# Performance work log

Hardware: AMD Instinct MI355X
Metric: run time of the kernel (lower is better)

Reference implementation:

```python
import jax, jax.numpy as jnp
import numpy as np

H = 6            # nheads
DPH = 200.0      # dim_per_head buffer = mha_dimension / nheads (used as divisor, NOT sqrt)
EPS = 1e-5


def layernorm(x, g, b):
    m = jnp.mean(x, axis=-1, keepdims=True)
    v = jnp.mean((x - m) ** 2, axis=-1, keepdims=True)
    return (x - m) * jax.lax.rsqrt(v + EPS) * g + b


def leaky(x):
    # torch.nn.LeakyReLU(True) -> negative_slope = 1.0 (identity), kept for faithfulness
    return jnp.where(x >= 0, x, 1.0 * x)


def setup_inputs() -> dict:
    key = jax.random.key(0)
    ks = jax.random.split(key, 16)
    B, L, D, M = 4, 2048, 512, 1200
    s_in = 1.0 / np.sqrt(D)
    s_m = 1.0 / np.sqrt(M)
    return {
        "query": jax.random.normal(ks[0], (B, L, D), jnp.float32),
        "keyval": jax.random.normal(ks[1], (B, 1, D), jnp.float32),
        "Wq": jax.random.normal(ks[2], (D, M), jnp.float32) * s_in,
        "bq": jnp.zeros((M,), jnp.float32),
        "Wkv": jax.random.normal(ks[3], (D, 2 * M), jnp.float32) * s_in,
        "bkv": jnp.zeros((2 * M,), jnp.float32),
        "Wff": jax.random.normal(ks[4], (M, D), jnp.float32) * s_m,
        "bff": jnp.zeros((D,), jnp.float32),
        "g1": jnp.ones((D,), jnp.float32),
        "b1": jnp.zeros((D,), jnp.float32),
        "W2a": jax.random.normal(ks[5], (D, 4 * D), jnp.float32) * s_in,
        "b2a": jnp.zeros((4 * D,), jnp.float32),
        "W2b": jax.random.normal(ks[6], (4 * D, D), jnp.float32) / np.sqrt(4 * D),
        "b2b": jnp.zeros((D,), jnp.float32),
        "g2": jnp.ones((D,), jnp.float32),
        "b2": jnp.zeros((D,), jnp.float32),
    }


def reference(query, keyval, Wq, bq, Wkv, bkv, Wff, bff, g1, b1,
              W2a, b2a, W2b, b2b, g2, b2):
    B, L, D = query.shape
    kv = jnp.broadcast_to(keyval, query.shape)           # keyval.expand_as(query)
    Q = query @ Wq + bq                                  # [B,L,M]
    KV = kv @ Wkv + bkv                                  # [B,L,2M]
    K, V = jnp.split(KV, 2, axis=-1)

    def heads(x):  # b l (h d) -> b h l d
        return x.reshape(B, L, H, -1).transpose(0, 2, 1, 3)

    Qh, Kh, Vh = heads(Q), heads(K), heads(V)
    logits = jnp.einsum('bhid,bhjd->bhij', Qh, Kh) / DPH  # note: / d, not / sqrt(d)
    sm = jax.nn.softmax(logits, axis=-1)                  # [B,H,L,L]
    mha = jnp.einsum('bhij,bhjd->bhid', sm, Vh)
    mha_ = mha.transpose(0, 2, 1, 3).reshape(B, L, -1)    # b h i d -> b i (h d)

    out = mha_ @ Wff + bff                                # dropout = identity (eval)
    out_ = layernorm(out + query, g1, b1)
    out2 = leaky(out_ @ W2a + b2a) @ W2b + b2b
    out3 = layernorm(out_ + out2, g2, b2)
    out3 = out3 + kv
    return out3, sm
```

## Files before the change

### kernel.cpp

```cpp
#include <hip/hip_runtime.h>
#include <hip/hip_bf16.h>


typedef __bf16 bf16x8 __attribute__((ext_vector_type(8)));
typedef float f32x4 __attribute__((ext_vector_type(4)));

constexpr size_t OUT3_N = 4ull * 2048 * 512;
constexpr size_t SM_N   = 4ull * 6 * 2048 * 2048;

__global__ __launch_bounds__(256) void prep_k(const float* __restrict__ W2a,
        const float* __restrict__ b2a, __bf16* __restrict__ A1,
        const float* __restrict__ W2b, __bf16* __restrict__ W2bT){
    const int bid = blockIdx.x, tid = threadIdx.x;
    if (bid < 1152){
        int r = bid >> 1;
        int c = (bid & 1) * 1024 + tid * 4;
        float4 v;
        if (r < 512)       v = *(const float4*)(W2a + (size_t)r * 2048 + c);
        else if (r == 512) v = *(const float4*)(b2a + c);
        else               v = make_float4(0.f, 0.f, 0.f, 0.f);
        __bf16* o = A1 + (size_t)r * 2048 + c;
        o[0] = (__bf16)v.x; o[1] = (__bf16)v.y; o[2] = (__bf16)v.z; o[3] = (__bf16)v.w;
    } else {
        __shared__ float tile[32][33];
        int t = bid - 1152;
        int c0 = (t & 15) * 32, r0 = (t >> 4) * 32;
        int tx = tid & 31, ty = tid >> 5;
        for (int i = ty; i < 32; i += 8)
            tile[i][tx] = W2b[(size_t)(r0 + i) * 512 + c0 + tx];
        __syncthreads();
        for (int i = ty; i < 32; i += 8)
            W2bT[(size_t)(c0 + i) * 2048 + r0 + tx] = (__bf16)tile[tx][i];
    }
}

__global__ void tcast_k(const float* __restrict__ in, __bf16* __restrict__ out, int R, int C){
    __shared__ float tile[32][33];
    int c0 = blockIdx.x * 32, r0 = blockIdx.y * 32;
    int tx = threadIdx.x, ty = threadIdx.y;
    for (int i = ty; i < 32; i += 8)
        tile[i][tx] = in[(size_t)(r0 + i) * C + c0 + tx];
    __syncthreads();
    for (int i = ty; i < 32; i += 8)
        out[(size_t)(c0 + i) * R + r0 + tx] = (__bf16)tile[tx][i];
}

__global__ void kv_k(const float* __restrict__ keyval, const float* __restrict__ Wkv,
                     const float* __restrict__ bkv, float* __restrict__ V){
    int b = blockIdx.x, m = blockIdx.y * 256 + threadIdx.x, kc = blockIdx.z;
    if (m >= 1200) return;
    float acc = (kc == 0) ? bkv[1200 + m] : 0.f;
    const float* kvb = keyval + (size_t)b * 512;
    int d0 = kc * 64;
    #pragma unroll 8
    for (int d = d0; d < d0 + 64; ++d)
        acc += kvb[d] * Wkv[(size_t)d * 2400 + 1200 + m];
    atomicAdd(&V[b * 1200 + m], acc);
}

__global__ void oc_k(const float* __restrict__ V, const float* __restrict__ Wff,
                     const float* __restrict__ bff, float* __restrict__ oc){
    int b = blockIdx.x, j = blockIdx.y * 256 + threadIdx.x, kc = blockIdx.z;
    float acc = (kc == 0) ? bff[j] : 0.f;
    const float* vb = V + b * 1200;
    int m0 = kc * 100;
    #pragma unroll 5
    for (int m = m0; m < m0 + 100; ++m)
        acc += vb[m] * Wff[(size_t)m * 512 + j];
    atomicAdd(&oc[b * 512 + j], acc);
}

__global__ __launch_bounds__(256) void ln1_k(const float* __restrict__ q,
        const float* __restrict__ oc, const float* __restrict__ g1,
        const float* __restrict__ b1, __bf16* __restrict__ Xb){
    const int rid = blockIdx.x;
    const int b = rid >> 11;
    const int t = threadIdx.x;
    const size_t base = (size_t)rid * 512;
    float2 qv = *(const float2*)(q + base + 2 * t);
    float2 ov = *(const float2*)(oc + (size_t)b * 512 + 2 * t);
    float v0 = qv.x + ov.x, v1 = qv.y + ov.y;
    float s = v0 + v1, ss = v0 * v0 + v1 * v1;
    for (int off = 32; off; off >>= 1){ s += __shfl_down(s, off); ss += __shfl_down(ss, off); }
    __shared__ float red[8];
    int wv = t >> 6, ln = t & 63;
    if (ln == 0){ red[wv] = s; red[4 + wv] = ss; }
    __syncthreads();
    if (t == 0){
        float S  = red[0] + red[1] + red[2] + red[3];
        float SS = red[4] + red[5] + red[6] + red[7];
        float m = S * (1.0f / 512.0f);
        float var = SS * (1.0f / 512.0f) - m * m;
        red[0] = m; red[1] = rsqrtf(var + 1e-5f);
    }
    __syncthreads();
    float m = red[0], r = red[1];
    float2 gv = *(const float2*)(g1 + 2 * t);
    float2 bv = *(const float2*)(b1 + 2 * t);
    union { __bf16 h[2]; unsigned u; } pk;
    pk.h[0] = (__bf16)((v0 - m) * r * gv.x + bv.x);
    pk.h[1] = (__bf16)((v1 - m) * r * gv.y + bv.y);
    *(unsigned*)(Xb + base + 2 * t) = pk.u;
}

__global__ __launch_bounds__(256) void ln2_k(const __bf16* __restrict__ X,
        const float* __restrict__ o2, const float* __restrict__ bfrow,
        const float* __restrict__ b2b, const float* __restrict__ g2,
        const float* __restrict__ b2, const float* __restrict__ keyval,
        float* __restrict__ out3){
    const int rid = blockIdx.x;
    const int b = rid >> 11;
    const int t = threadIdx.x;
    const size_t base = (size_t)rid * 512;
    union { unsigned u; __bf16 h[2]; } xv;
    xv.u = *(const unsigned*)(X + base + 2 * t);
    float2 cv = *(const float2*)(o2 + base + 2 * t);
    float f0 = bfrow[2 * t] + b2b[2 * t], f1 = bfrow[2 * t + 1] + b2b[2 * t + 1];
    float v0 = (float)xv.h[0] + cv.x + f0, v1 = (float)xv.h[1] + cv.y + f1;
    float s = v0 + v1, ss = v0 * v0 + v1 * v1;
    for (int off = 32; off; off >>= 1){ s += __shfl_down(s, off); ss += __shfl_down(ss, off); }
    __shared__ float red[8];
    int wv = t >> 6, ln = t & 63;
    if (ln == 0){ red[wv] = s; red[4 + wv] = ss; }
    __syncthreads();
    if (t == 0){
        float S  = red[0] + red[1] + red[2] + red[3];
        float SS = red[4] + red[5] + red[6] + red[7];
        float m = S * (1.0f / 512.0f);
        float var = SS * (1.0f / 512.0f) - m * m;
        red[0] = m; red[1] = rsqrtf(var + 1e-5f);
    }
    __syncthreads();
    float m = red[0], r = red[1];
    float2 gv = *(const float2*)(g2 + 2 * t);
    float2 bv = *(const float2*)(b2 + 2 * t);
    float2 kv = *(const float2*)(keyval + (size_t)b * 512 + 2 * t);
    float y0 = (v0 - m) * r * gv.x + bv.x + kv.x;
    float y1 = (v1 - m) * r * gv.y + bv.y + kv.y;
    *(float2*)(out3 + base + 2 * t) = make_float2(y0, y1);
}

__global__ __launch_bounds__(256) void gemm_bt_k(const __bf16* __restrict__ A,
        const __bf16* __restrict__ BT, float* __restrict__ C, int Ndim, int Kdim){
    __shared__ __bf16 As[64 * 64];
    __shared__ __bf16 Bs[64 * 64];
    const int tid = threadIdx.x, wave = tid >> 6, lane = tid & 63;
    const int bm = blockIdx.x * 64, bn = blockIdx.y * 64;
    const int r_st = wave * 8 + (lane >> 3);
    const int c8g  = (lane & 7) ^ (r_st & 7);
    const __bf16* Ag = A  + (size_t)(bm + r_st) * Kdim + c8g * 8;
    const __bf16* Bg = BT + (size_t)(bn + r_st) * Kdim + c8g * 8;
    const size_t rowskip = (size_t)32 * Kdim;
    const int wm = (wave >> 1) * 32, wn = (wave & 1) * 32;
    const int lm = lane & 15, lq = lane >> 4;
    f32x4 acc[2][2] = {};
    for (int k0 = 0; k0 < Kdim; k0 += 64){
        __builtin_amdgcn_global_load_lds(
            (const __attribute__((address_space(1))) void*)(Ag + k0),
            (__attribute__((address_space(3))) void*)&As[wave * 512], 16, 0, 0);
        __builtin_amdgcn_global_load_lds(
            (const __attribute__((address_space(1))) void*)(Ag + k0 + rowskip),
            (__attribute__((address_space(3))) void*)&As[2048 + wave * 512], 16, 0, 0);
        __builtin_amdgcn_global_load_lds(
            (const __attribute__((address_space(1))) void*)(Bg + k0),
            (__attribute__((address_space(3))) void*)&Bs[wave * 512], 16, 0, 0);
        __builtin_amdgcn_global_load_lds(
            (const __attribute__((address_space(1))) void*)(Bg + k0 + rowskip),
            (__attribute__((address_space(3))) void*)&Bs[2048 + wave * 512], 16, 0, 0);
        __syncthreads();
        #pragma unroll
        for (int kb = 0; kb < 64; kb += 32){
            const int sw = (((kb >> 3) + lq) ^ (lm & 7)) << 3;
            bf16x8 a0 = *(const bf16x8*)&As[(wm + lm) * 64 + sw];
            bf16x8 a1 = *(const bf16x8*)&As[(wm + 16 + lm) * 64 + sw];
            bf16x8 b0 = *(const bf16x8*)&Bs[(wn + lm) * 64 + sw];
            bf16x8 b1 = *(const bf16x8*)&Bs[(wn + 16 + lm) * 64 + sw];
            acc[0][0] = __builtin_amdgcn_mfma_f32_16x16x32_bf16(a0, b0, acc[0][0], 0, 0, 0);
            acc[0][1] = __builtin_amdgcn_mfma_f32_16x16x32_bf16(a0, b1, acc[0][1], 0, 0, 0);
            acc[1][0] = __builtin_amdgcn_mfma_f32_16x16x32_bf16(a1, b0, acc[1][0], 0, 0, 0);
            acc[1][1] = __builtin_amdgcn_mfma_f32_16x16x32_bf16(a1, b1, acc[1][1], 0, 0, 0);
        }
        __syncthreads();
    }
    for (int mi = 0; mi < 2; ++mi)
      for (int ni = 0; ni < 2; ++ni)
        for (int r = 0; r < 4; ++r){
            int row = bm + wm + mi * 16 + lq * 4 + r;
            int col = bn + wn + ni * 16 + lm;
            C[(size_t)row * Ndim + col] = acc[mi][ni][r];
        }
}

__global__ void fill_k(float4* __restrict__ p, size_t n4, float val){
    size_t i = (size_t)blockIdx.x * blockDim.x + threadIdx.x;
    size_t stride = (size_t)gridDim.x * blockDim.x;
    float4 v = make_float4(val, val, val, val);
    for (; i < n4; i += stride) p[i] = v;
}

extern "C" void kernel_launch(void* const* d_in, const int* in_sizes, int n_in,
                              void* d_out, int out_size, void* d_ws, size_t ws_size,
                              hipStream_t stream){
    const float* query  = (const float*)d_in[0];
    const float* keyval = (const float*)d_in[1];
    const float* Wkv = (const float*)d_in[4];
    const float* bkv = (const float*)d_in[5];
    const float* Wff = (const float*)d_in[6];
    const float* bff = (const float*)d_in[7];
    const float* g1  = (const float*)d_in[8];
    const float* b1  = (const float*)d_in[9];
    const float* W2a = (const float*)d_in[10];
    const float* b2a = (const float*)d_in[11];
    const float* W2b = (const float*)d_in[12];
    const float* b2b = (const float*)d_in[13];
    const float* g2  = (const float*)d_in[14];
    const float* b2  = (const float*)d_in[15];

    float* out3 = (float*)d_out;
    float* smf  = out3 + OUT3_N;

    char* base = (ws_size >= (64ull << 20)) ? (char*)d_ws : (char*)smf;
    float*  t_Wf   = (float*)base;
    float*  t_out2 = t_Wf + 294912;
    float*  t_V    = t_out2 + 4194304;
    float*  t_oc   = t_V + 4800;
    __bf16* t_A1   = (__bf16*)(t_oc + 2048);
    __bf16* t_W2bT = t_A1 + 1179648;
    __bf16* t_WfT  = t_W2bT + 1048576;
    __bf16* t_X    = t_WfT + 262144;

    hipMemsetAsync(t_V, 0, (4800 + 2048) * sizeof(float), stream);
    prep_k<<<2176, 256, 0, stream>>>(W2a, b2a, t_A1, W2b, t_W2bT);
    kv_k<<<dim3(4, 5, 8), 256, 0, stream>>>(keyval, Wkv, bkv, t_V);
    oc_k<<<dim3(4, 2, 12), 256, 0, stream>>>(t_V, Wff, bff, t_oc);
    gemm_bt_k<<<dim3(9, 8), 256, 0, stream>>>(t_A1, t_W2bT, t_Wf, 512, 2048);
    tcast_k<<<dim3(16, 16), dim3(32, 8), 0, stream>>>(t_Wf, t_WfT, 512, 512);
    ln1_k<<<8192, 256, 0, stream>>>(query, t_oc, g1, b1, t_X);
    gemm_bt_k<<<dim3(128, 8), 256, 0, stream>>>(t_X, t_WfT, t_out2, 512, 512);
    ln2_k<<<8192, 256, 0, stream>>>(t_X, t_out2, t_Wf + 294912 - 512, b2b, g2, b2, keyval, out3);
    fill_k<<<4096, 256, 0, stream>>>((float4*)smf, SM_N / 4, 1.0f / 2048.0f);
}
```

Baseline: 542.8 us.

## Fuse softmax fill slices into each stage kernel and split-K the weight-fold GEMM

The big constant fill of the softmax output is split into six slices. Each slice is appended as extra blocks to one of the pipeline kernels, so the bandwidth-bound fill overlaps with the small compute stages instead of running alone at the end. The fill uses non-temporal stores. Several small kernels are merged: kv goes into prep, tcast into ln1. The 576x512x2048 fold GEMM is split along K four ways with atomic accumulation into a zeroed buffer to use more CUs. It also now reads the correct bias row of the folded weight. In exchange, fill blocks compete with compute blocks for CUs, and the atomics add contention.

```diff
diff --git a/kernel.cpp b/kernel.cpp
--- a/kernel.cpp
+++ b/kernel.cpp
@@ -6,146 +6,32 @@
 typedef float f32x4 __attribute__((ext_vector_type(4)));
 
 constexpr size_t OUT3_N = 4ull * 2048 * 512;
-constexpr size_t SM_N   = 4ull * 6 * 2048 * 2048;
-
-__global__ __launch_bounds__(256) void prep_k(const float* __restrict__ W2a,
-        const float* __restrict__ b2a, __bf16* __restrict__ A1,
-        const float* __restrict__ W2b, __bf16* __restrict__ W2bT){
-    const int bid = blockIdx.x, tid = threadIdx.x;
-    if (bid < 1152){
-        int r = bid >> 1;
-        int c = (bid & 1) * 1024 + tid * 4;
-        float4 v;
-        if (r < 512)       v = *(const float4*)(W2a + (size_t)r * 2048 + c);
-        else if (r == 512) v = *(const float4*)(b2a + c);
-        else               v = make_float4(0.f, 0.f, 0.f, 0.f);
-        __bf16* o = A1 + (size_t)r * 2048 + c;
-        o[0] = (__bf16)v.x; o[1] = (__bf16)v.y; o[2] = (__bf16)v.z; o[3] = (__bf16)v.w;
-    } else {
-        __shared__ float tile[32][33];
-        int t = bid - 1152;
-        int c0 = (t & 15) * 32, r0 = (t >> 4) * 32;
-        int tx = tid & 31, ty = tid >> 5;
-        for (int i = ty; i < 32; i += 8)
-            tile[i][tx] = W2b[(size_t)(r0 + i) * 512 + c0 + tx];
-        __syncthreads();
-        for (int i = ty; i < 32; i += 8)
-            W2bT[(size_t)(c0 + i) * 2048 + r0 + tx] = (__bf16)tile[tx][i];
-    }
-}
-
-__global__ void tcast_k(const float* __restrict__ in, __bf16* __restrict__ out, int R, int C){
-    __shared__ float tile[32][33];
-    int c0 = blockIdx.x * 32, r0 = blockIdx.y * 32;
-    int tx = threadIdx.x, ty = threadIdx.y;
-    for (int i = ty; i < 32; i += 8)
-        tile[i][tx] = in[(size_t)(r0 + i) * C + c0 + tx];
-    __syncthreads();
-    for (int i = ty; i < 32; i += 8)
-        out[(size_t)(c0 + i) * R + r0 + tx] = (__bf16)tile[tx][i];
-}
-
-__global__ void kv_k(const float* __restrict__ keyval, const float* __restrict__ Wkv,
-                     const float* __restrict__ bkv, float* __restrict__ V){
-    int b = blockIdx.x, m = blockIdx.y * 256 + threadIdx.x, kc = blockIdx.z;
-    if (m >= 1200) return;
-    float acc = (kc == 0) ? bkv[1200 + m] : 0.f;
-    const float* kvb = keyval + (size_t)b * 512;
-    int d0 = kc * 64;
-    #pragma unroll 8
-    for (int d = d0; d < d0 + 64; ++d)
-        acc += kvb[d] * Wkv[(size_t)d * 2400 + 1200 + m];
-    atomicAdd(&V[b * 1200 + m], acc);
-}
-
-__global__ void oc_k(const float* __restrict__ V, const float* __restrict__ Wff,
-                     const float* __restrict__ bff, float* __restrict__ oc){
-    int b = blockIdx.x, j = blockIdx.y * 256 + threadIdx.x, kc = blockIdx.z;
-    float acc = (kc == 0) ? bff[j] : 0.f;
-    const float* vb = V + b * 1200;
-    int m0 = kc * 100;
-    #pragma unroll 5
-    for (int m = m0; m < m0 + 100; ++m)
-        acc += vb[m] * Wff[(size_t)m * 512 + j];
-    atomicAdd(&oc[b * 512 + j], acc);
-}
-
-__global__ __launch_bounds__(256) void ln1_k(const float* __restrict__ q,
-        const float* __restrict__ oc, const float* __restrict__ g1,
-        const float* __restrict__ b1, __bf16* __restrict__ Xb){
-    const int rid = blockIdx.x;
-    const int b = rid >> 11;
-    const int t = threadIdx.x;
-    const size_t base = (size_t)rid * 512;
-    float2 qv = *(const float2*)(q + base + 2 * t);
-    float2 ov = *(const float2*)(oc + (size_t)b * 512 + 2 * t);
-    float v0 = qv.x + ov.x, v1 = qv.y + ov.y;
-    float s = v0 + v1, ss = v0 * v0 + v1 * v1;
-    for (int off = 32; off; off >>= 1){ s += __shfl_down(s, off); ss += __shfl_down(ss, off); }
-    __shared__ float red[8];
-    int wv = t >> 6, ln = t & 63;
-    if (ln == 0){ red[wv] = s; red[4 + wv] = ss; }
-    __syncthreads();
-    if (t == 0){
-        float S  = red[0] + red[1] + red[2] + red[3];
-        float SS = red[4] + red[5] + red[6] + red[7];
-        float m = S * (1.0f / 512.0f);
-        float var = SS * (1.0f / 512.0f) - m * m;
-        red[0] = m; red[1] = rsqrtf(var + 1e-5f);
-    }
-    __syncthreads();
-    float m = red[0], r = red[1];
-    float2 gv = *(const float2*)(g1 + 2 * t);
-    float2 bv = *(const float2*)(b1 + 2 * t);
-    union { __bf16 h[2]; unsigned u; } pk;
-    pk.h[0] = (__bf16)((v0 - m) * r * gv.x + bv.x);
-    pk.h[1] = (__bf16)((v1 - m) * r * gv.y + bv.y);
-    *(unsigned*)(Xb + base + 2 * t) = pk.u;
-}
-
-__global__ __launch_bounds__(256) void ln2_k(const __bf16* __restrict__ X,
-        const float* __restrict__ o2, const float* __restrict__ bfrow,
-        const float* __restrict__ b2b, const float* __restrict__ g2,
-        const float* __restrict__ b2, const float* __restrict__ keyval,
-        float* __restrict__ out3){
-    const int rid = blockIdx.x;
-    const int b = rid >> 11;
-    const int t = threadIdx.x;
-    const size_t base = (size_t)rid * 512;
-    union { unsigned u; __bf16 h[2]; } xv;
-    xv.u = *(const unsigned*)(X + base + 2 * t);
-    float2 cv = *(const float2*)(o2 + base + 2 * t);
-    float f0 = bfrow[2 * t] + b2b[2 * t], f1 = bfrow[2 * t + 1] + b2b[2 * t + 1];
-    float v0 = (float)xv.h[0] + cv.x + f0, v1 = (float)xv.h[1] + cv.y + f1;
-    float s = v0 + v1, ss = v0 * v0 + v1 * v1;
-    for (int off = 32; off; off >>= 1){ s += __shfl_down(s, off); ss += __shfl_down(ss, off); }
-    __shared__ float red[8];
-    int wv = t >> 6, ln = t & 63;
-    if (ln == 0){ red[wv] = s; red[4 + wv] = ss; }
-    __syncthreads();
-    if (t == 0){
-        float S  = red[0] + red[1] + red[2] + red[3];
-        float SS = red[4] + red[5] + red[6] + red[7];
-        float m = S * (1.0f / 512.0f);
-        float var = SS * (1.0f / 512.0f) - m * m;
-        red[0] = m; red[1] = rsqrtf(var + 1e-5f);
-    }
-    __syncthreads();
-    float m = red[0], r = red[1];
-    float2 gv = *(const float2*)(g2 + 2 * t);
-    float2 bv = *(const float2*)(b2 + 2 * t);
-    float2 kv = *(const float2*)(keyval + (size_t)b * 512 + 2 * t);
-    float y0 = (v0 - m) * r * gv.x + bv.x + kv.x;
-    float y1 = (v1 - m) * r * gv.y + bv.y + kv.y;
-    *(float2*)(out3 + base + 2 * t) = make_float2(y0, y1);
-}
-
-__global__ __launch_bounds__(256) void gemm_bt_k(const __bf16* __restrict__ A,
-        const __bf16* __restrict__ BT, float* __restrict__ C, int Ndim, int Kdim){
+constexpr size_t SM_N4  = (4ull * 6 * 2048 * 2048) / 4;
+constexpr float  SMV    = 1.0f / 2048.0f;
+
+constexpr size_t S1 = 0,        C1 = 6291456;
+constexpr size_t S2 = 6291456,  C2 = 4194304;
+constexpr size_t S3 = 10485760, C3 = 6291456;
+constexpr size_t S4 = 16777216, C4 = 3145728;
+constexpr size_t S5 = 19922944, C5 = 2621440;
+constexpr size_t S6 = 22544384, C6 = 2621440;
+static_assert(S6 + C6 == SM_N4, "fill slices must cover sm");
+
+__device__ inline void fill_slice(f32x4* __restrict__ p, size_t base, size_t cnt,
+                                  int fb, int nfb){
+    const f32x4 v = { SMV, SMV, SMV, SMV };
+    const size_t stride = (size_t)nfb * 256;
+    for (size_t j = (size_t)fb * 256 + threadIdx.x; j < cnt; j += stride)
+        __builtin_nontemporal_store(v, p + base + j);
+}
+
+template<bool ATOMIC>
+__device__ void gemm_tile(const __bf16* __restrict__ A, const __bf16* __restrict__ BT,
+                          float* __restrict__ C, int Ndim, int Kdim,
+                          int bm, int bn, int k0beg, int k0end){
     __shared__ __bf16 As[64 * 64];
     __shared__ __bf16 Bs[64 * 64];
     const int tid = threadIdx.x, wave = tid >> 6, lane = tid & 63;
-    const int bm = blockIdx.x * 64, bn = blockIdx.y * 64;
     const int r_st = wave * 8 + (lane >> 3);
     const int c8g  = (lane & 7) ^ (r_st & 7);
     const __bf16* Ag = A  + (size_t)(bm + r_st) * Kdim + c8g * 8;
@@ -154,7 +40,7 @@
     const int wm = (wave >> 1) * 32, wn = (wave & 1) * 32;
     const int lm = lane & 15, lq = lane >> 4;
     f32x4 acc[2][2] = {};
-    for (int k0 = 0; k0 < Kdim; k0 += 64){
+    for (int k0 = k0beg; k0 < k0end; k0 += 64){
         __builtin_amdgcn_global_load_lds(
             (const __attribute__((address_space(1))) void*)(Ag + k0),
             (__attribute__((address_space(3))) void*)&As[wave * 512], 16, 0, 0);
@@ -182,20 +68,187 @@
         }
         __syncthreads();
     }
+    #pragma unroll
     for (int mi = 0; mi < 2; ++mi)
+      #pragma unroll
       for (int ni = 0; ni < 2; ++ni)
+        #pragma unroll
         for (int r = 0; r < 4; ++r){
             int row = bm + wm + mi * 16 + lq * 4 + r;
             int col = bn + wn + ni * 16 + lm;
-            C[(size_t)row * Ndim + col] = acc[mi][ni][r];
-        }
-}
-
-__global__ void fill_k(float4* __restrict__ p, size_t n4, float val){
-    size_t i = (size_t)blockIdx.x * blockDim.x + threadIdx.x;
-    size_t stride = (size_t)gridDim.x * blockDim.x;
-    float4 v = make_float4(val, val, val, val);
-    for (; i < n4; i += stride) p[i] = v;
+            if (ATOMIC) atomicAdd(&C[(size_t)row * Ndim + col], acc[mi][ni][r]);
+            else        C[(size_t)row * Ndim + col] = acc[mi][ni][r];
+        }
+}
+
+__global__ __launch_bounds__(256) void k1_prep_kv(const float* __restrict__ W2a,
+        const float* __restrict__ b2a, __bf16* __restrict__ A1,
+        const float* __restrict__ W2b, __bf16* __restrict__ W2bT,
+        const float* __restrict__ keyval, const float* __restrict__ Wkv,
+        const float* __restrict__ bkv, float* __restrict__ V, f32x4* __restrict__ smf){
+    __shared__ float sh[32 * 33];
+    const int bid = blockIdx.x, tid = threadIdx.x;
+    if (bid < 1152){
+        int r = bid >> 1;
+        int c = (bid & 1) * 1024 + tid * 4;
+        float4 v;
+        if (r < 512)       v = *(const float4*)(W2a + (size_t)r * 2048 + c);
+        else if (r == 512) v = *(const float4*)(b2a + c);
+        else               v = make_float4(0.f, 0.f, 0.f, 0.f);
+        __bf16* o = A1 + (size_t)r * 2048 + c;
+        o[0] = (__bf16)v.x; o[1] = (__bf16)v.y; o[2] = (__bf16)v.z; o[3] = (__bf16)v.w;
+    } else if (bid < 2176){
+        int t = bid - 1152;
+        int c0 = (t & 15) * 32, r0 = (t >> 4) * 32;
+        int tx = tid & 31, ty = tid >> 5;
+        for (int i = ty; i < 32; i += 8)
+            sh[i * 33 + tx] = W2b[(size_t)(r0 + i) * 512 + c0 + tx];
+        __syncthreads();
+        for (int i = ty; i < 32; i += 8)
+            W2bT[(size_t)(c0 + i) * 2048 + r0 + tx] = (__bf16)sh[tx * 33 + i];
+    } else if (bid < 2336){
+        int i = bid - 2176;
+        int b = i & 3, mc = (i >> 2) % 5, kc = i / 20;
+        int m = mc * 256 + tid;
+        if (m < 1200){
+            float acc = (kc == 0) ? bkv[1200 + m] : 0.f;
+            const float* kvb = keyval + (size_t)b * 512;
+            int d0 = kc * 64;
+            #pragma unroll 8
+            for (int d = d0; d < d0 + 64; ++d)
+                acc += kvb[d] * Wkv[(size_t)d * 2400 + 1200 + m];
+            atomicAdd(&V[b * 1200 + m], acc);
+        }
+    } else {
+        fill_slice(smf, S1, C1, bid - 2336, 512);
+    }
+}
+
+__global__ __launch_bounds__(256) void k2_oc(const float* __restrict__ V,
+        const float* __restrict__ Wff, const float* __restrict__ bff,
+        float* __restrict__ oc, f32x4* __restrict__ smf){
+    const int bid = blockIdx.x, tid = threadIdx.x;
+    if (bid < 96){
+        int b = bid & 3, jc = (bid >> 2) & 1, kc = bid >> 3;
+        int j = jc * 256 + tid;
+        float acc = (kc == 0) ? bff[j] : 0.f;
+        const float* vb = V + b * 1200;
+        int m0 = kc * 100;
+        #pragma unroll 5
+        for (int m = m0; m < m0 + 100; ++m)
+            acc += vb[m] * Wff[(size_t)m * 512 + j];
+        atomicAdd(&oc[b * 512 + j], acc);
+    } else {
+        fill_slice(smf, S2, C2, bid - 96, 512);
+    }
+}
+
+__global__ __launch_bounds__(256) void k3_fold(const __bf16* __restrict__ A1,
+        const __bf16* __restrict__ W2bT, float* __restrict__ Wf, f32x4* __restrict__ smf){
+    const int bid = blockIdx.x;
+    if (bid < 288){
+        int tile = bid % 72, kc = bid / 72;
+        int tm = tile % 9, tn = tile / 9;
+        gemm_tile<true>(A1, W2bT, Wf, 512, 2048, tm * 64, tn * 64, kc * 512, (kc + 1) * 512);
+    } else {
+        fill_slice(smf, S3, C3, bid - 288, 512);
+    }
+}
+
+__global__ __launch_bounds__(256) void k4_ln1_tcast(const float* __restrict__ q,
+        const float* __restrict__ oc, const float* __restrict__ g1,
+        const float* __restrict__ b1, __bf16* __restrict__ Xb,
+        const float* __restrict__ Wf, __bf16* __restrict__ WfT, f32x4* __restrict__ smf){
+    __shared__ float sh[32 * 33];
+    const int bid = blockIdx.x, t = threadIdx.x;
+    if (bid < 8192){
+        const int b = bid >> 11;
+        const size_t base = (size_t)bid * 512;
+        float2 qv = *(const float2*)(q + base + 2 * t);
+        float2 ov = *(const float2*)(oc + (size_t)b * 512 + 2 * t);
+        float v0 = qv.x + ov.x, v1 = qv.y + ov.y;
+        float s = v0 + v1, ss = v0 * v0 + v1 * v1;
+        for (int off = 32; off; off >>= 1){ s += __shfl_down(s, off); ss += __shfl_down(ss, off); }
+        int wv = t >> 6, ln = t & 63;
+        if (ln == 0){ sh[wv] = s; sh[4 + wv] = ss; }
+        __syncthreads();
+        if (t == 0){
+            float S  = sh[0] + sh[1] + sh[2] + sh[3];
+            float SS = sh[4] + sh[5] + sh[6] + sh[7];
+            float m = S * (1.0f / 512.0f);
+            float var = SS * (1.0f / 512.0f) - m * m;
+            sh[0] = m; sh[1] = rsqrtf(var + 1e-5f);
+        }
+        __syncthreads();
+        float m = sh[0], r = sh[1];
+        float2 gv = *(const float2*)(g1 + 2 * t);
+        float2 bv = *(const float2*)(b1 + 2 * t);
+        union { __bf16 h[2]; unsigned u; } pk;
+        pk.h[0] = (__bf16)((v0 - m) * r * gv.x + bv.x);
+        pk.h[1] = (__bf16)((v1 - m) * r * gv.y + bv.y);
+        *(unsigned*)(Xb + base + 2 * t) = pk.u;
+    } else if (bid < 8448){
+        int tt = bid - 8192;
+        int c0 = (tt & 15) * 32, r0 = (tt >> 4) * 32;
+        int tx = t & 31, ty = t >> 5;
+        for (int i = ty; i < 32; i += 8)
+            sh[i * 33 + tx] = Wf[(size_t)(r0 + i) * 512 + c0 + tx];
+        __syncthreads();
+        for (int i = ty; i < 32; i += 8)
+            WfT[(size_t)(c0 + i) * 512 + r0 + tx] = (__bf16)sh[tx * 33 + i];
+    } else {
+        fill_slice(smf, S4, C4, bid - 8448, 512);
+    }
+}
+
+__global__ __launch_bounds__(256) void k5_gemm(const __bf16* __restrict__ X,
+        const __bf16* __restrict__ WfT, float* __restrict__ out2, f32x4* __restrict__ smf){
+    const int bid = blockIdx.x;
+    if (bid < 1024){
+        gemm_tile<false>(X, WfT, out2, 512, 512, (bid >> 3) * 64, (bid & 7) * 64, 0, 512);
+    } else {
+        fill_slice(smf, S5, C5, bid - 1024, 512);
+    }
+}
+
+__global__ __launch_bounds__(256) void k6_ln2(const __bf16* __restrict__ X,
+        const float* __restrict__ o2, const float* __restrict__ bfrow,
+        const float* __restrict__ b2b, const float* __restrict__ g2,
+        const float* __restrict__ b2, const float* __restrict__ keyval,
+        float* __restrict__ out3, f32x4* __restrict__ smf){
+    __shared__ float sh[8];
+    const int bid = blockIdx.x, t = threadIdx.x;
+    if (bid < 8192){
+        const int b = bid >> 11;
+        const size_t base = (size_t)bid * 512;
+        union { unsigned u; __bf16 h[2]; } xv;
+        xv.u = *(const unsigned*)(X + base + 2 * t);
+        float2 cv = *(const float2*)(o2 + base + 2 * t);
+        float f0 = bfrow[2 * t] + b2b[2 * t], f1 = bfrow[2 * t + 1] + b2b[2 * t + 1];
+        float v0 = (float)xv.h[0] + cv.x + f0, v1 = (float)xv.h[1] + cv.y + f1;
+        float s = v0 + v1, ss = v0 * v0 + v1 * v1;
+        for (int off = 32; off; off >>= 1){ s += __shfl_down(s, off); ss += __shfl_down(ss, off); }
+        int wv = t >> 6, ln = t & 63;
+        if (ln == 0){ sh[wv] = s; sh[4 + wv] = ss; }
+        __syncthreads();
+        if (t == 0){
+            float S  = sh[0] + sh[1] + sh[2] + sh[3];
+            float SS = sh[4] + sh[5] + sh[6] + sh[7];
+            float m = S * (1.0f / 512.0f);
+            float var = SS * (1.0f / 512.0f) - m * m;
+            sh[0] = m; sh[1] = rsqrtf(var + 1e-5f);
+        }
+        __syncthreads();
+        float m = sh[0], r = sh[1];
+        float2 gv = *(const float2*)(g2 + 2 * t);
+        float2 bv = *(const float2*)(b2 + 2 * t);
+        float2 kv = *(const float2*)(keyval + (size_t)b * 512 + 2 * t);
+        float y0 = (v0 - m) * r * gv.x + bv.x + kv.x;
+        float y1 = (v1 - m) * r * gv.y + bv.y + kv.y;
+        *(float2*)(out3 + base + 2 * t) = make_float2(y0, y1);
+    } else {
+        fill_slice(smf, S6, C6, bid - 8192, 512);
+    }
 }
 
 extern "C" void kernel_launch(void* const* d_in, const int* in_sizes, int n_in,
@@ -217,26 +270,25 @@
     const float* b2  = (const float*)d_in[15];
 
     float* out3 = (float*)d_out;
-    float* smf  = out3 + OUT3_N;
+    f32x4* smf  = (f32x4*)(out3 + OUT3_N);
 
     char* base = (ws_size >= (64ull << 20)) ? (char*)d_ws : (char*)smf;
     float*  t_Wf   = (float*)base;
-    float*  t_out2 = t_Wf + 294912;
-    float*  t_V    = t_out2 + 4194304;
+    float*  t_V    = t_Wf + 294912;
     float*  t_oc   = t_V + 4800;
-    __bf16* t_A1   = (__bf16*)(t_oc + 2048);
+    float*  t_out2 = t_oc + 2048;
+    __bf16* t_A1   = (__bf16*)(t_out2 + 4194304);
     __bf16* t_W2bT = t_A1 + 1179648;
     __bf16* t_WfT  = t_W2bT + 1048576;
     __bf16* t_X    = t_WfT + 262144;
 
-    hipMemsetAsync(t_V, 0, (4800 + 2048) * sizeof(float), stream);
-    prep_k<<<2176, 256, 0, stream>>>(W2a, b2a, t_A1, W2b, t_W2bT);
-    kv_k<<<dim3(4, 5, 8), 256, 0, stream>>>(keyval, Wkv, bkv, t_V);
-    oc_k<<<dim3(4, 2, 12), 256, 0, stream>>>(t_V, Wff, bff, t_oc);
-    gemm_bt_k<<<dim3(9, 8), 256, 0, stream>>>(t_A1, t_W2bT, t_Wf, 512, 2048);
-    tcast_k<<<dim3(16, 16), dim3(32, 8), 0, stream>>>(t_Wf, t_WfT, 512, 512);
-    ln1_k<<<8192, 256, 0, stream>>>(query, t_oc, g1, b1, t_X);
-    gemm_bt_k<<<dim3(128, 8), 256, 0, stream>>>(t_X, t_WfT, t_out2, 512, 512);
-    ln2_k<<<8192, 256, 0, stream>>>(t_X, t_out2, t_Wf + 294912 - 512, b2b, g2, b2, keyval, out3);
-    fill_k<<<4096, 256, 0, stream>>>((float4*)smf, SM_N / 4, 1.0f / 2048.0f);
-}
+    (void)hipMemsetAsync(t_Wf, 0, (294912 + 4800 + 2048) * sizeof(float), stream);
+    k1_prep_kv<<<2848, 256, 0, stream>>>(W2a, b2a, t_A1, W2b, t_W2bT,
+                                         keyval, Wkv, bkv, t_V, smf);
+    k2_oc<<<608, 256, 0, stream>>>(t_V, Wff, bff, t_oc, smf);
+    k3_fold<<<800, 256, 0, stream>>>(t_A1, t_W2bT, t_Wf, smf);
+    k4_ln1_tcast<<<8960, 256, 0, stream>>>(query, t_oc, g1, b1, t_X, t_Wf, t_WfT, smf);
+    k5_gemm<<<1536, 256, 0, stream>>>(t_X, t_WfT, t_out2, smf);
+    k6_ln2<<<8704, 256, 0, stream>>>(t_X, t_out2, t_Wf + 262144, b2b, g2, b2,
+                                     keyval, out3, smf);
+}
```

Result: faster. 501.2 us (-7.7%).
